# Kernel tuning notes

Hardware: AMD Instinct MI355X
Metric: run time of the kernel (lower is better)

The kernel has to match this reference:

```python
import jax, jax.numpy as jnp
import numpy as np

N_NODES = 50000
N_EDGES = 1600000
N_GRAPHS = 512
HID = 64


def _mlp_params(key, din, dout, scale=0.1):
    k1, k2, k3 = jax.random.split(key, 3)
    return (
        jax.random.normal(k1, (din, HID), jnp.float32) * scale, jnp.zeros((HID,), jnp.float32),
        jax.random.normal(k2, (HID, HID), jnp.float32) * scale, jnp.zeros((HID,), jnp.float32),
        jax.random.normal(k3, (HID, dout), jnp.float32) * scale, jnp.zeros((dout,), jnp.float32),
    )


def _mlp(x, w1, b1, w2, b2, w3, b3, out_act=None):
    h = jax.nn.relu(x @ w1 + b1)
    h = jax.nn.relu(h @ w2 + b2)
    o = h @ w3 + b3
    return o if out_act is None else out_act(o)


def setup_inputs() -> dict:
    key = jax.random.key(0)
    ks = jax.random.split(key, 8)
    nf = jax.random.normal(ks[0], (N_NODES, 1), jnp.float32)
    ef = jax.random.normal(ks[1], (N_EDGES, 1), jnp.float32)
    src = jax.random.randint(ks[2], (N_EDGES,), 0, N_NODES)
    dst = jax.random.randint(ks[3], (N_EDGES,), 0, N_NODES)
    graph_id = jnp.sort(jax.random.randint(ks[4], (N_NODES,), 0, N_GRAPHS))
    e_w1, e_b1, e_w2, e_b2, e_w3, e_b3 = _mlp_params(ks[5], 3, 1)   # edge model: [src_nf, dst_nf, ef] -> msg
    n_w1, n_b1, n_w2, n_b2, n_w3, n_b3 = _mlp_params(ks[6], 2, 1)   # node model: [nf, agg] -> unf
    m_w1, m_b1, m_w2, m_b2, m_w3, m_b3 = _mlp_params(ks[7], 1, 1)   # node-wise MLP with Sigmoid out_act
    return dict(nf=nf, ef=ef, src=src, dst=dst, graph_id=graph_id,
                e_w1=e_w1, e_b1=e_b1, e_w2=e_w2, e_b2=e_b2, e_w3=e_w3, e_b3=e_b3,
                n_w1=n_w1, n_b1=n_b1, n_w2=n_w2, n_b2=n_b2, n_w3=n_w3, n_b3=n_b3,
                m_w1=m_w1, m_b1=m_b1, m_w2=m_w2, m_b2=m_b2, m_w3=m_w3, m_b3=m_b3)


def reference(nf, ef, src, dst, graph_id,
              e_w1, e_b1, e_w2, e_b2, e_w3, e_b3,
              n_w1, n_b1, n_w2, n_b2, n_w3, n_b3,
              m_w1, m_b1, m_w2, m_b2, m_w3, m_b3):
    # MPNN layer: message on edges, sum-aggregate to dst nodes, node update
    em_in = jnp.concatenate([nf[src], nf[dst], ef], axis=-1)          # [E, 3]
    msg = _mlp(em_in, e_w1, e_b1, e_w2, e_b2, e_w3, e_b3)             # [E, 1]
    agg = jax.ops.segment_sum(msg, dst, num_segments=N_NODES)        # [N, 1]
    unf = _mlp(jnp.concatenate([nf, agg], axis=-1),
               n_w1, n_b1, n_w2, n_b2, n_w3, n_b3)                    # [N, 1]
    # node-wise MLP with Sigmoid output activation
    node_out = _mlp(unf, m_w1, m_b1, m_w2, m_b2, m_w3, m_b3,
                    out_act=jax.nn.sigmoid)                           # [N, 1]
    # sum readout per graph, then final sigmoid
    rd = jax.ops.segment_sum(node_out, graph_id, num_segments=N_GRAPHS)  # [G, 1]
    return jax.nn.sigmoid(rd)
```

## Files before the change

### kernel.cpp

```cpp
#include <hip/hip_runtime.h>
#include <math.h>

#define HID 64
#define BKT_SHIFT 13
#define BKT_RANGE 8192
#define CCHUNK 32

typedef __attribute__((ext_vector_type(8))) short short8;
typedef __attribute__((ext_vector_type(4))) float f32x4;
typedef unsigned long long ull;

union FragU {
    uint4 q;
    short8 v;
    uint32_t u[4];
};

__device__ __forceinline__ uint32_t cvt_pk_bf16(float lo, float hi) {
    uint32_t r;
    asm("v_cvt_pk_bf16_f32 %0, %1, %2" : "=v"(r) : "v"(lo), "v"(hi));
    return r;
}

__global__ __launch_bounds__(256) void edge_mlp_kernel(
    const float* __restrict__ nf, const float* __restrict__ ef,
    const int* __restrict__ src, const int* __restrict__ dst,
    const float* __restrict__ w1, const float* __restrict__ b1,
    const float* __restrict__ w2, const float* __restrict__ b2,
    const float* __restrict__ w3, const float* __restrict__ b3,
    uint2* __restrict__ recs, ull* __restrict__ offs,
    float* __restrict__ aggFb, int E, int B, int mode)
{
    __shared__ uint4 hbuf[256 * 8];

    const int tid  = threadIdx.x;
    const int lane = tid & 63;
    const int wid  = tid >> 6;
    const int g    = lane >> 4;
    const int eL   = lane & 15;

    FragU af[4][2];
#pragma unroll
    for (int t = 0; t < 4; ++t)
#pragma unroll
        for (int h = 0; h < 2; ++h)
#pragma unroll
            for (int e2 = 0; e2 < 4; ++e2) {
                int k0 = h * 32 + g * 8 + 2 * e2;
                float v0 = w2[(k0    ) * HID + t * 16 + eL];
                float v1 = w2[(k0 + 1) * HID + t * 16 + eL];
                af[t][h].u[e2] = cvt_pk_bf16(v0, v1);
            }

    float b2v[16], w3v[16];
#pragma unroll
    for (int t = 0; t < 4; ++t)
#pragma unroll
        for (int r = 0; r < 4; ++r) {
            int j = t * 16 + g * 4 + r;
            b2v[t * 4 + r] = b2[j];
            w3v[t * 4 + r] = w3[j];
        }
    const float b3c = b3[0];

    const int e0 = blockIdx.x * 256;
    const int eidx = e0 + tid;
    const int ei = eidx < E ? eidx : E - 1;
    const int dmine = dst[ei];
    {
        float a = nf[src[ei]];
        float b = nf[dmine];
        float c = ef[ei];

        uint32_t pk[32];
#pragma unroll
        for (int k2 = 0; k2 < 32; ++k2) {
            int k0 = 2 * k2, k1 = 2 * k2 + 1;
            float h0 = fmaxf(fmaf(a, w1[k0], fmaf(b, w1[HID + k0], fmaf(c, w1[2 * HID + k0], b1[k0]))), 0.f);
            float h1 = fmaxf(fmaf(a, w1[k1], fmaf(b, w1[HID + k1], fmaf(c, w1[2 * HID + k1], b1[k1]))), 0.f);
            pk[k2] = cvt_pk_bf16(h0, h1);
        }

        uint4* rowp = &hbuf[tid * 8];
        int sw = tid & 7;
#pragma unroll
        for (int ch = 0; ch < 8; ++ch)
            rowp[ch ^ sw] = make_uint4(pk[4 * ch], pk[4 * ch + 1], pk[4 * ch + 2], pk[4 * ch + 3]);
    }

    float mymsg = 0.f;

#pragma unroll
    for (int s = 0; s < 4; ++s) {
        int row = wid * 64 + s * 16 + eL;
        int sw  = lane & 7;
        FragU bf0, bf1;
        bf0.q = hbuf[row * 8 + ((    g) ^ sw)];
        bf1.q = hbuf[row * 8 + ((4 + g) ^ sw)];

        f32x4 ac[4];
#pragma unroll
        for (int t = 0; t < 4; ++t) {
            ac[t][0] = b2v[t * 4 + 0];
            ac[t][1] = b2v[t * 4 + 1];
            ac[t][2] = b2v[t * 4 + 2];
            ac[t][3] = b2v[t * 4 + 3];
            ac[t] = __builtin_amdgcn_mfma_f32_16x16x32_bf16(af[t][0].v, bf0.v, ac[t], 0, 0, 0);
            ac[t] = __builtin_amdgcn_mfma_f32_16x16x32_bf16(af[t][1].v, bf1.v, ac[t], 0, 0, 0);
        }

        float p = 0.f;
#pragma unroll
        for (int t = 0; t < 4; ++t)
#pragma unroll
            for (int r = 0; r < 4; ++r)
                p = fmaf(fmaxf(ac[t][r], 0.f), w3v[t * 4 + r], p);

        p += __shfl_xor(p, 16);
        p += __shfl_xor(p, 32);

        if (s == (lane >> 4)) mymsg = p + b3c;
    }

    const bool valid = eidx < E;

    if (mode == 1) {
        if (valid) atomicAdd(&aggFb[dmine], mymsg);
        return;
    }

    const int bkt = dmine >> BKT_SHIFT;
    const ull lt = (1ull << lane) - 1;
    int myslot = 0;
    int off = 0;
    uint32_t pack_lo = 0, pack_hi = 0;
    for (int b = 0; b < B; ++b) {
        if (b < 4) pack_lo |= (uint32_t)off << (8 * b);
        else       pack_hi |= (uint32_t)off << (8 * (b - 4));
        ull m = __ballot(valid && bkt == b);
        if (valid && bkt == b) myslot = off + (int)__popcll(m & lt);
        off += (int)__popcll(m);
    }
    pack_hi |= (uint32_t)off << 24;

    const size_t wgl = (size_t)blockIdx.x * 4 + wid;
    if (valid) recs[wgl * 64 + myslot] = make_uint2((uint32_t)dmine, __float_as_uint(mymsg));
    if (lane == 0) offs[wgl] = ((ull)pack_hi << 32) | (ull)pack_lo;
}

__global__ __launch_bounds__(256) void bucket_accum_kernel(
    const uint2* __restrict__ recs, const ull* __restrict__ offs,
    float* __restrict__ partial, int NW, int B)
{
    __shared__ float acc[BKT_RANGE];

    const int b = blockIdx.x / CCHUNK;
    const int c = blockIdx.x % CCHUNK;

    for (int i = threadIdx.x; i < BKT_RANGE; i += 256) acc[i] = 0.f;
    __syncthreads();

    const int wpc = (NW + CCHUNK - 1) / CCHUNK;
    const int w0 = c * wpc;
    const int w1 = (w0 + wpc < NW) ? w0 + wpc : NW;
    const int nb = b + 1;
    const int base_node = b << BKT_SHIFT;

    for (int w = w0 + threadIdx.x; w < w1; w += 256) {
        ull ov = offs[w];
        uint32_t lo = (uint32_t)ov, hi = (uint32_t)(ov >> 32);
        int ob = (int)(((b  < 4) ? (lo >> (8 * b))        : (hi >> (8 * (b  - 4)))) & 0xFF);
        int oe = (int)(((nb < 4) ? (lo >> (8 * nb))       : (hi >> (8 * (nb - 4)))) & 0xFF);
        const uint2* rb = recs + (size_t)w * 64;
        for (int r = ob; r < oe; ++r) {
            uint2 rec = rb[r];
            atomicAdd(&acc[(int)rec.x - base_node], __uint_as_float(rec.y));
        }
    }
    __syncthreads();

    float* pb = partial + ((size_t)b * CCHUNK + c) * BKT_RANGE;
    for (int i = threadIdx.x; i < BKT_RANGE; i += 256) pb[i] = acc[i];
}

__global__ __launch_bounds__(256) void bucket_reduce_kernel(
    const float* __restrict__ partial, float* __restrict__ agg, int N)
{
    int n = blockIdx.x * 256 + threadIdx.x;
    if (n >= N) return;
    int b = n >> BKT_SHIFT, nl = n & (BKT_RANGE - 1);
    const float* p = partial + (size_t)b * CCHUNK * BKT_RANGE + nl;
    float s = 0.f;
#pragma unroll 8
    for (int c = 0; c < CCHUNK; ++c) s += p[(size_t)c * BKT_RANGE];
    agg[n] = s;
}

__global__ __launch_bounds__(64) void node_mfma_kernel(
    const float* __restrict__ nf, const float* __restrict__ agg,
    const int* __restrict__ gid,
    const float* __restrict__ nw1, const float* __restrict__ nb1,
    const float* __restrict__ nw2, const float* __restrict__ nb2,
    const float* __restrict__ nw3, const float* __restrict__ nb3,
    const float* __restrict__ mw1, const float* __restrict__ mb1,
    const float* __restrict__ mw2, const float* __restrict__ mb2,
    const float* __restrict__ mw3, const float* __restrict__ mb3,
    float* __restrict__ rd, int N)
{
    __shared__ uint4 hbuf[64 * 8];
    __shared__ float unfbuf[64];
    __shared__ float obuf[64];

    const int lane = threadIdx.x;
    const int g    = lane >> 4;
    const int eL   = lane & 15;
    const int sw   = lane & 7;

    const int base = blockIdx.x * 64;
    const int idx  = base + lane;
    const int i    = idx < N ? idx : N - 1;
    const float x0 = nf[i];
    const float x1 = agg[i];

    {
        uint32_t pk[32];
#pragma unroll
        for (int k2 = 0; k2 < 32; ++k2) {
            int k0 = 2 * k2, k1 = 2 * k2 + 1;
            float h0 = fmaxf(fmaf(x0, nw1[k0], fmaf(x1, nw1[HID + k0], nb1[k0])), 0.f);
            float h1 = fmaxf(fmaf(x0, nw1[k1], fmaf(x1, nw1[HID + k1], nb1[k1])), 0.f);
            pk[k2] = cvt_pk_bf16(h0, h1);
        }
        uint4* rowp = &hbuf[lane * 8];
#pragma unroll
        for (int ch = 0; ch < 8; ++ch)
            rowp[ch ^ sw] = make_uint4(pk[4 * ch], pk[4 * ch + 1], pk[4 * ch + 2], pk[4 * ch + 3]);

        FragU af[4][2];
#pragma unroll
        for (int t = 0; t < 4; ++t)
#pragma unroll
            for (int h = 0; h < 2; ++h)
#pragma unroll
                for (int e2 = 0; e2 < 4; ++e2) {
                    int k0 = h * 32 + g * 8 + 2 * e2;
                    float v0 = nw2[(k0    ) * HID + t * 16 + eL];
                    float v1 = nw2[(k0 + 1) * HID + t * 16 + eL];
                    af[t][h].u[e2] = cvt_pk_bf16(v0, v1);
                }
        float b2v[16], w3v[16];
#pragma unroll
        for (int t = 0; t < 4; ++t)
#pragma unroll
            for (int r = 0; r < 4; ++r) {
                int j = t * 16 + g * 4 + r;
                b2v[t * 4 + r] = nb2[j];
                w3v[t * 4 + r] = nw3[j];
            }
        const float b3c = nb3[0];

#pragma unroll
        for (int s = 0; s < 4; ++s) {
            int row = s * 16 + eL;
            FragU bf0, bf1;
            bf0.q = hbuf[row * 8 + ((    g) ^ (row & 7))];
            bf1.q = hbuf[row * 8 + ((4 + g) ^ (row & 7))];

            f32x4 ac[4];
#pragma unroll
            for (int t = 0; t < 4; ++t) {
                ac[t][0] = b2v[t * 4 + 0];
                ac[t][1] = b2v[t * 4 + 1];
                ac[t][2] = b2v[t * 4 + 2];
                ac[t][3] = b2v[t * 4 + 3];
                ac[t] = __builtin_amdgcn_mfma_f32_16x16x32_bf16(af[t][0].v, bf0.v, ac[t], 0, 0, 0);
                ac[t] = __builtin_amdgcn_mfma_f32_16x16x32_bf16(af[t][1].v, bf1.v, ac[t], 0, 0, 0);
            }

            float p = 0.f;
#pragma unroll
            for (int t = 0; t < 4; ++t)
#pragma unroll
                for (int r = 0; r < 4; ++r)
                    p = fmaf(fmaxf(ac[t][r], 0.f), w3v[t * 4 + r], p);

            p += __shfl_xor(p, 16);
            p += __shfl_xor(p, 32);

            if (lane < 16)
                unfbuf[s * 16 + lane] = p + b3c;
        }
    }

    const float unf = unfbuf[lane];

    {
        uint32_t pk[32];
#pragma unroll
        for (int k2 = 0; k2 < 32; ++k2) {
            int k0 = 2 * k2, k1 = 2 * k2 + 1;
            float h0 = fmaxf(fmaf(unf, mw1[k0], mb1[k0]), 0.f);
            float h1 = fmaxf(fmaf(unf, mw1[k1], mb1[k1]), 0.f);
            pk[k2] = cvt_pk_bf16(h0, h1);
        }
        uint4* rowp = &hbuf[lane * 8];
#pragma unroll
        for (int ch = 0; ch < 8; ++ch)
            rowp[ch ^ sw] = make_uint4(pk[4 * ch], pk[4 * ch + 1], pk[4 * ch + 2], pk[4 * ch + 3]);

        FragU af[4][2];
#pragma unroll
        for (int t = 0; t < 4; ++t)
#pragma unroll
            for (int h = 0; h < 2; ++h)
#pragma unroll
                for (int e2 = 0; e2 < 4; ++e2) {
                    int k0 = h * 32 + g * 8 + 2 * e2;
                    float v0 = mw2[(k0    ) * HID + t * 16 + eL];
                    float v1 = mw2[(k0 + 1) * HID + t * 16 + eL];
                    af[t][h].u[e2] = cvt_pk_bf16(v0, v1);
                }
        float b2v[16], w3v[16];
#pragma unroll
        for (int t = 0; t < 4; ++t)
#pragma unroll
            for (int r = 0; r < 4; ++r) {
                int j = t * 16 + g * 4 + r;
                b2v[t * 4 + r] = mb2[j];
                w3v[t * 4 + r] = mw3[j];
            }
        const float b3c = mb3[0];

#pragma unroll
        for (int s = 0; s < 4; ++s) {
            int row = s * 16 + eL;
            FragU bf0, bf1;
            bf0.q = hbuf[row * 8 + ((    g) ^ (row & 7))];
            bf1.q = hbuf[row * 8 + ((4 + g) ^ (row & 7))];

            f32x4 ac[4];
#pragma unroll
            for (int t = 0; t < 4; ++t) {
                ac[t][0] = b2v[t * 4 + 0];
                ac[t][1] = b2v[t * 4 + 1];
                ac[t][2] = b2v[t * 4 + 2];
                ac[t][3] = b2v[t * 4 + 3];
                ac[t] = __builtin_amdgcn_mfma_f32_16x16x32_bf16(af[t][0].v, bf0.v, ac[t], 0, 0, 0);
                ac[t] = __builtin_amdgcn_mfma_f32_16x16x32_bf16(af[t][1].v, bf1.v, ac[t], 0, 0, 0);
            }

            float p = 0.f;
#pragma unroll
            for (int t = 0; t < 4; ++t)
#pragma unroll
                for (int r = 0; r < 4; ++r)
                    p = fmaf(fmaxf(ac[t][r], 0.f), w3v[t * 4 + r], p);

            p += __shfl_xor(p, 16);
            p += __shfl_xor(p, 32);

            if (lane < 16) {
                float o = p + b3c;
                obuf[s * 16 + lane] = 1.0f / (1.0f + expf(-o));
            }
        }
    }

    {
        const bool ok = idx < N;
        float v = ok ? obuf[lane] : 0.0f;
        int   gg = gid[i];

#pragma unroll
        for (int d = 1; d < 64; d <<= 1) {
            float vup = __shfl_up(v, d);
            int   gup = __shfl_up(gg, d);
            if (lane >= d && gup == gg) v += vup;
        }
        int gdn = __shfl_down(gg, 1);
        bool tail = (lane == 63) || (gdn != gg);
        if (tail)
            atomicAdd(&rd[gg], v);
    }
}

__global__ void readout_kernel(const float* __restrict__ rd,
                               float* __restrict__ out, int G)
{
    int g = blockIdx.x * blockDim.x + threadIdx.x;
    if (g < G) out[g] = 1.0f / (1.0f + expf(-rd[g]));
}

extern "C" void kernel_launch(void* const* d_in, const int* in_sizes, int n_in,
                              void* d_out, int out_size, void* d_ws, size_t ws_size,
                              hipStream_t stream)
{
    const float* nf  = (const float*)d_in[0];
    const float* ef  = (const float*)d_in[1];
    const int*   src = (const int*)  d_in[2];
    const int*   dst = (const int*)  d_in[3];
    const int*   gid = (const int*)  d_in[4];

    const float* e_w1 = (const float*)d_in[5];
    const float* e_b1 = (const float*)d_in[6];
    const float* e_w2 = (const float*)d_in[7];
    const float* e_b2 = (const float*)d_in[8];
    const float* e_w3 = (const float*)d_in[9];
    const float* e_b3 = (const float*)d_in[10];

    const float* n_w1 = (const float*)d_in[11];
    const float* n_b1 = (const float*)d_in[12];
    const float* n_w2 = (const float*)d_in[13];
    const float* n_b2 = (const float*)d_in[14];
    const float* n_w3 = (const float*)d_in[15];
    const float* n_b3 = (const float*)d_in[16];

    const float* m_w1 = (const float*)d_in[17];
    const float* m_b1 = (const float*)d_in[18];
    const float* m_w2 = (const float*)d_in[19];
    const float* m_b2 = (const float*)d_in[20];
    const float* m_w3 = (const float*)d_in[21];
    const float* m_b3 = (const float*)d_in[22];

    const int N = in_sizes[0];
    const int E = in_sizes[2];
    const int G = out_size;

    const int NW = (E + 63) / 64;
    const int B  = (N + BKT_RANGE - 1) / BKT_RANGE;

    size_t recs_b   = (size_t)NW * 64 * sizeof(uint2);
    size_t offs_b   = (size_t)NW * sizeof(ull);
    size_t part_b   = (size_t)B * CCHUNK * BKT_RANGE * sizeof(float);
    size_t need     = recs_b + offs_b + part_b + ((size_t)N + G) * sizeof(float);
    bool   bucketok = (B <= 8) && (need <= ws_size);

    float* out = (float*)d_out;

    if (bucketok) {
        uint2* recs    = (uint2*)d_ws;
        ull*   offs    = (ull*)((char*)d_ws + recs_b);
        float* partial = (float*)((char*)d_ws + recs_b + offs_b);
        float* agg     = (float*)((char*)d_ws + recs_b + offs_b + part_b);
        float* rd      = agg + N;

        hipMemsetAsync(rd, 0, (size_t)G * sizeof(float), stream);

        edge_mlp_kernel<<<(E + 255) / 256, 256, 0, stream>>>(
            nf, ef, src, dst, e_w1, e_b1, e_w2, e_b2, e_w3, e_b3,
            recs, offs, nullptr, E, B, 0);

        bucket_accum_kernel<<<B * CCHUNK, 256, 0, stream>>>(
            recs, offs, partial, NW, B);

        bucket_reduce_kernel<<<(N + 255) / 256, 256, 0, stream>>>(
            partial, agg, N);

        node_mfma_kernel<<<(N + 63) / 64, 64, 0, stream>>>(
            nf, agg, gid,
            n_w1, n_b1, n_w2, n_b2, n_w3, n_b3,
            m_w1, m_b1, m_w2, m_b2, m_w3, m_b3,
            rd, N);

        readout_kernel<<<(G + 255) / 256, 256, 0, stream>>>(rd, out, G);
    } else {
        float* agg = (float*)d_ws;
        float* rd  = agg + N;

        hipMemsetAsync(d_ws, 0, ((size_t)N + G) * sizeof(float), stream);

        edge_mlp_kernel<<<(E + 255) / 256, 256, 0, stream>>>(
            nf, ef, src, dst, e_w1, e_b1, e_w2, e_b2, e_w3, e_b3,
            nullptr, nullptr, agg, E, B, 1);

        node_mfma_kernel<<<(N + 63) / 64, 64, 0, stream>>>(
            nf, agg, gid,
            n_w1, n_b1, n_w2, n_b2, n_w3, n_b3,
            m_w1, m_b1, m_w2, m_b2, m_w3, m_b3,
            rd, N);

        readout_kernel<<<(G + 255) / 256, 256, 0, stream>>>(rd, out, G);
    }
}
```

Baseline: 85.85 us.

## Compute first MLP layer with MFMA and prepack bf16 weights in a prep kernel

```diff
diff --git a/kernel.cpp b/kernel.cpp
--- a/kernel.cpp
+++ b/kernel.cpp
@@ -21,17 +21,47 @@
     asm("v_cvt_pk_bf16_f32 %0, %1, %2" : "=v"(r) : "v"(lo), "v"(hi));
     return r;
 }
-
-__global__ __launch_bounds__(256) void edge_mlp_kernel(
+__device__ __forceinline__ float bf16lo_f(uint32_t u) { return __uint_as_float(u << 16); }
+__device__ __forceinline__ float bf16hi_f(uint32_t u) { return __uint_as_float(u & 0xFFFF0000u); }
+__device__ __forceinline__ unsigned short bf16_of(float v) {
+    return (unsigned short)(cvt_pk_bf16(v, 0.f) & 0xFFFFu);
+}
+
+__global__ void prep_kernel(
+    const float* __restrict__ w1,  const float* __restrict__ b1,  const float* __restrict__ w2,
+    const float* __restrict__ nw1, const float* __restrict__ nb1, const float* __restrict__ nw2,
+    const float* __restrict__ mw1, const float* __restrict__ mb1, const float* __restrict__ mw2,
+    unsigned short* __restrict__ w1x,  unsigned short* __restrict__ w2T,
+    unsigned short* __restrict__ nw1x, unsigned short* __restrict__ nw2T,
+    unsigned short* __restrict__ mw1x, unsigned short* __restrict__ mw2T)
+{
+    int t = blockIdx.x * 256 + threadIdx.x;
+    if (t < 4096) {
+        int j = t >> 6, k = t & 63;
+        w2T [t] = bf16_of(w2 [k * HID + j]);
+        nw2T[t] = bf16_of(nw2[k * HID + j]);
+        mw2T[t] = bf16_of(mw2[k * HID + j]);
+    }
+    if (t < 512) {
+        int j = t >> 3, k = t & 7;
+        float ve = k == 0 ? w1[j] : k == 1 ? w1[HID + j] : k == 2 ? w1[2 * HID + j] : k == 3 ? b1[j] : 0.f;
+        float vn = k == 0 ? nw1[j] : k == 1 ? nw1[HID + j] : k == 2 ? nb1[j] : 0.f;
+        float vm = k == 0 ? mw1[j] : k == 1 ? mb1[j] : 0.f;
+        w1x [t] = bf16_of(ve);
+        nw1x[t] = bf16_of(vn);
+        mw1x[t] = bf16_of(vm);
+    }
+}
+
+__global__ __launch_bounds__(256, 4) void edge_mfma2_kernel(
     const float* __restrict__ nf, const float* __restrict__ ef,
     const int* __restrict__ src, const int* __restrict__ dst,
-    const float* __restrict__ w1, const float* __restrict__ b1,
-    const float* __restrict__ w2, const float* __restrict__ b2,
-    const float* __restrict__ w3, const float* __restrict__ b3,
+    const unsigned short* __restrict__ w1x, const unsigned short* __restrict__ w2T,
+    const float* __restrict__ b2, const float* __restrict__ w3, const float* __restrict__ b3,
     uint2* __restrict__ recs, ull* __restrict__ offs,
     float* __restrict__ aggFb, int E, int B, int mode)
 {
-    __shared__ uint4 hbuf[256 * 8];
+    __shared__ uint2 tile[4][16][16];
 
     const int tid  = threadIdx.x;
     const int lane = tid & 63;
@@ -39,87 +69,80 @@
     const int g    = lane >> 4;
     const int eL   = lane & 15;
 
-    FragU af[4][2];
+    FragU af1[4];
+#pragma unroll
+    for (int t = 0; t < 4; ++t) {
+        uint4 q = *(const uint4*)&w1x[(t * 16 + eL) * 8];
+        af1[t].q = (g == 0) ? q : make_uint4(0, 0, 0, 0);
+    }
+    FragU af2[4][2];
 #pragma unroll
     for (int t = 0; t < 4; ++t)
 #pragma unroll
         for (int h = 0; h < 2; ++h)
-#pragma unroll
-            for (int e2 = 0; e2 < 4; ++e2) {
-                int k0 = h * 32 + g * 8 + 2 * e2;
-                float v0 = w2[(k0    ) * HID + t * 16 + eL];
-                float v1 = w2[(k0 + 1) * HID + t * 16 + eL];
-                af[t][h].u[e2] = cvt_pk_bf16(v0, v1);
-            }
-
-    float b2v[16], w3v[16];
-#pragma unroll
-    for (int t = 0; t < 4; ++t)
-#pragma unroll
-        for (int r = 0; r < 4; ++r) {
-            int j = t * 16 + g * 4 + r;
-            b2v[t * 4 + r] = b2[j];
-            w3v[t * 4 + r] = w3[j];
-        }
+            af2[t][h].q = *(const uint4*)&w2T[(t * 16 + eL) * 64 + h * 32 + g * 8];
+
+    f32x4 b2v4[4];
+    uint32_t w3p[8];
+#pragma unroll
+    for (int t = 0; t < 4; ++t) {
+        int j = t * 16 + g * 4;
+        b2v4[t] = *(const f32x4*)&b2[j];
+        f32x4 wv = *(const f32x4*)&w3[j];
+        w3p[2 * t]     = cvt_pk_bf16(wv[0], wv[1]);
+        w3p[2 * t + 1] = cvt_pk_bf16(wv[2], wv[3]);
+    }
     const float b3c = b3[0];
 
-    const int e0 = blockIdx.x * 256;
+    const int e0   = blockIdx.x * 256;
     const int eidx = e0 + tid;
-    const int ei = eidx < E ? eidx : E - 1;
+    const int ei   = eidx < E ? eidx : E - 1;
     const int dmine = dst[ei];
-    {
-        float a = nf[src[ei]];
-        float b = nf[dmine];
-        float c = ef[ei];
-
-        uint32_t pk[32];
-#pragma unroll
-        for (int k2 = 0; k2 < 32; ++k2) {
-            int k0 = 2 * k2, k1 = 2 * k2 + 1;
-            float h0 = fmaxf(fmaf(a, w1[k0], fmaf(b, w1[HID + k0], fmaf(c, w1[2 * HID + k0], b1[k0]))), 0.f);
-            float h1 = fmaxf(fmaf(a, w1[k1], fmaf(b, w1[HID + k1], fmaf(c, w1[2 * HID + k1], b1[k1]))), 0.f);
-            pk[k2] = cvt_pk_bf16(h0, h1);
-        }
-
-        uint4* rowp = &hbuf[tid * 8];
-        int sw = tid & 7;
-#pragma unroll
-        for (int ch = 0; ch < 8; ++ch)
-            rowp[ch ^ sw] = make_uint4(pk[4 * ch], pk[4 * ch + 1], pk[4 * ch + 2], pk[4 * ch + 3]);
-    }
+    const float a = nf[src[ei]];
+    const float b = nf[dmine];
+    const float c = ef[ei];
 
     float mymsg = 0.f;
 
 #pragma unroll
     for (int s = 0; s < 4; ++s) {
-        int row = wid * 64 + s * 16 + eL;
-        int sw  = lane & 7;
+        float av = __shfl(a, s * 16 + eL);
+        float bv = __shfl(b, s * 16 + eL);
+        float cv = __shfl(c, s * 16 + eL);
+        FragU bin;
+        bin.u[0] = (g == 0) ? cvt_pk_bf16(av, bv) : 0u;
+        bin.u[1] = (g == 0) ? cvt_pk_bf16(cv, 1.0f) : 0u;
+        bin.u[2] = 0u; bin.u[3] = 0u;
+
+#pragma unroll
+        for (int t = 0; t < 4; ++t) {
+            f32x4 h4 = __builtin_amdgcn_mfma_f32_16x16x32_bf16(
+                af1[t].v, bin.v, (f32x4){0.f, 0.f, 0.f, 0.f}, 0, 0, 0);
+            uint32_t p0 = cvt_pk_bf16(fmaxf(h4[0], 0.f), fmaxf(h4[1], 0.f));
+            uint32_t p1 = cvt_pk_bf16(fmaxf(h4[2], 0.f), fmaxf(h4[3], 0.f));
+            tile[wid][eL][(4 * t + g) ^ ((eL & 7) << 1)] = make_uint2(p0, p1);
+        }
+
         FragU bf0, bf1;
-        bf0.q = hbuf[row * 8 + ((    g) ^ sw)];
-        bf1.q = hbuf[row * 8 + ((4 + g) ^ sw)];
-
-        f32x4 ac[4];
-#pragma unroll
-        for (int t = 0; t < 4; ++t) {
-            ac[t][0] = b2v[t * 4 + 0];
-            ac[t][1] = b2v[t * 4 + 1];
-            ac[t][2] = b2v[t * 4 + 2];
-            ac[t][3] = b2v[t * 4 + 3];
-            ac[t] = __builtin_amdgcn_mfma_f32_16x16x32_bf16(af[t][0].v, bf0.v, ac[t], 0, 0, 0);
-            ac[t] = __builtin_amdgcn_mfma_f32_16x16x32_bf16(af[t][1].v, bf1.v, ac[t], 0, 0, 0);
+        {
+            const uint4* row = (const uint4*)&tile[wid][eL][0];
+            bf0.q = row[(g)     ^ (eL & 7)];
+            bf1.q = row[(4 + g) ^ (eL & 7)];
         }
 
         float p = 0.f;
 #pragma unroll
-        for (int t = 0; t < 4; ++t)
-#pragma unroll
-            for (int r = 0; r < 4; ++r)
-                p = fmaf(fmaxf(ac[t][r], 0.f), w3v[t * 4 + r], p);
-
+        for (int t = 0; t < 4; ++t) {
+            f32x4 ac = __builtin_amdgcn_mfma_f32_16x16x32_bf16(af2[t][0].v, bf0.v, b2v4[t], 0, 0, 0);
+            ac = __builtin_amdgcn_mfma_f32_16x16x32_bf16(af2[t][1].v, bf1.v, ac, 0, 0, 0);
+            p = fmaf(fmaxf(ac[0], 0.f), bf16lo_f(w3p[2 * t]),     p);
+            p = fmaf(fmaxf(ac[1], 0.f), bf16hi_f(w3p[2 * t]),     p);
+            p = fmaf(fmaxf(ac[2], 0.f), bf16lo_f(w3p[2 * t + 1]), p);
+            p = fmaf(fmaxf(ac[3], 0.f), bf16hi_f(w3p[2 * t + 1]), p);
+        }
         p += __shfl_xor(p, 16);
         p += __shfl_xor(p, 32);
-
-        if (s == (lane >> 4)) mymsg = p + b3c;
+        if (s == g) mymsg = p + b3c;
     }
 
     const bool valid = eidx < E;
@@ -169,8 +192,8 @@
     for (int w = w0 + threadIdx.x; w < w1; w += 256) {
         ull ov = offs[w];
         uint32_t lo = (uint32_t)ov, hi = (uint32_t)(ov >> 32);
-        int ob = (int)(((b  < 4) ? (lo >> (8 * b))        : (hi >> (8 * (b  - 4)))) & 0xFF);
-        int oe = (int)(((nb < 4) ? (lo >> (8 * nb))       : (hi >> (8 * (nb - 4)))) & 0xFF);
+        int ob = (int)(((b  < 4) ? (lo >> (8 * b))  : (hi >> (8 * (b  - 4)))) & 0xFF);
+        int oe = (int)(((nb < 4) ? (lo >> (8 * nb)) : (hi >> (8 * (nb - 4)))) & 0xFF);
         const uint2* rb = recs + (size_t)w * 64;
         for (int r = ob; r < oe; ++r) {
             uint2 rec = rb[r];
@@ -196,191 +219,143 @@
     agg[n] = s;
 }
 
-__global__ __launch_bounds__(64) void node_mfma_kernel(
+__global__ __launch_bounds__(64, 2) void node_mfma2_kernel(
     const float* __restrict__ nf, const float* __restrict__ agg,
     const int* __restrict__ gid,
-    const float* __restrict__ nw1, const float* __restrict__ nb1,
-    const float* __restrict__ nw2, const float* __restrict__ nb2,
-    const float* __restrict__ nw3, const float* __restrict__ nb3,
-    const float* __restrict__ mw1, const float* __restrict__ mb1,
-    const float* __restrict__ mw2, const float* __restrict__ mb2,
-    const float* __restrict__ mw3, const float* __restrict__ mb3,
+    const unsigned short* __restrict__ nw1x, const unsigned short* __restrict__ nw2T,
+    const float* __restrict__ nb2, const float* __restrict__ nw3, const float* __restrict__ nb3,
+    const unsigned short* __restrict__ mw1x, const unsigned short* __restrict__ mw2T,
+    const float* __restrict__ mb2, const float* __restrict__ mw3, const float* __restrict__ mb3,
     float* __restrict__ rd, int N)
 {
-    __shared__ uint4 hbuf[64 * 8];
-    __shared__ float unfbuf[64];
-    __shared__ float obuf[64];
+    __shared__ uint2 tile[16][16];
 
     const int lane = threadIdx.x;
     const int g    = lane >> 4;
     const int eL   = lane & 15;
-    const int sw   = lane & 7;
-
-    const int base = blockIdx.x * 64;
-    const int idx  = base + lane;
-    const int i    = idx < N ? idx : N - 1;
-    const float x0 = nf[i];
-    const float x1 = agg[i];
+
+    const int n0 = blockIdx.x * 16;
+    const int nn = n0 + eL < N ? n0 + eL : N - 1;
+    const float x0 = nf[nn];
+    const float x1 = agg[nn];
+
+    float unf, o;
 
     {
-        uint32_t pk[32];
-#pragma unroll
-        for (int k2 = 0; k2 < 32; ++k2) {
-            int k0 = 2 * k2, k1 = 2 * k2 + 1;
-            float h0 = fmaxf(fmaf(x0, nw1[k0], fmaf(x1, nw1[HID + k0], nb1[k0])), 0.f);
-            float h1 = fmaxf(fmaf(x0, nw1[k1], fmaf(x1, nw1[HID + k1], nb1[k1])), 0.f);
-            pk[k2] = cvt_pk_bf16(h0, h1);
-        }
-        uint4* rowp = &hbuf[lane * 8];
-#pragma unroll
-        for (int ch = 0; ch < 8; ++ch)
-            rowp[ch ^ sw] = make_uint4(pk[4 * ch], pk[4 * ch + 1], pk[4 * ch + 2], pk[4 * ch + 3]);
-
-        FragU af[4][2];
-#pragma unroll
-        for (int t = 0; t < 4; ++t)
+        FragU af1[4], af2[4][2];
+        f32x4 b2v4[4]; uint32_t w3p[8];
+#pragma unroll
+        for (int t = 0; t < 4; ++t) {
+            uint4 q = *(const uint4*)&nw1x[(t * 16 + eL) * 8];
+            af1[t].q = (g == 0) ? q : make_uint4(0, 0, 0, 0);
 #pragma unroll
             for (int h = 0; h < 2; ++h)
-#pragma unroll
-                for (int e2 = 0; e2 < 4; ++e2) {
-                    int k0 = h * 32 + g * 8 + 2 * e2;
-                    float v0 = nw2[(k0    ) * HID + t * 16 + eL];
-                    float v1 = nw2[(k0 + 1) * HID + t * 16 + eL];
-                    af[t][h].u[e2] = cvt_pk_bf16(v0, v1);
-                }
-        float b2v[16], w3v[16];
-#pragma unroll
-        for (int t = 0; t < 4; ++t)
-#pragma unroll
-            for (int r = 0; r < 4; ++r) {
-                int j = t * 16 + g * 4 + r;
-                b2v[t * 4 + r] = nb2[j];
-                w3v[t * 4 + r] = nw3[j];
-            }
-        const float b3c = nb3[0];
-
-#pragma unroll
-        for (int s = 0; s < 4; ++s) {
-            int row = s * 16 + eL;
-            FragU bf0, bf1;
-            bf0.q = hbuf[row * 8 + ((    g) ^ (row & 7))];
-            bf1.q = hbuf[row * 8 + ((4 + g) ^ (row & 7))];
-
-            f32x4 ac[4];
-#pragma unroll
-            for (int t = 0; t < 4; ++t) {
-                ac[t][0] = b2v[t * 4 + 0];
-                ac[t][1] = b2v[t * 4 + 1];
-                ac[t][2] = b2v[t * 4 + 2];
-                ac[t][3] = b2v[t * 4 + 3];
-                ac[t] = __builtin_amdgcn_mfma_f32_16x16x32_bf16(af[t][0].v, bf0.v, ac[t], 0, 0, 0);
-                ac[t] = __builtin_amdgcn_mfma_f32_16x16x32_bf16(af[t][1].v, bf1.v, ac[t], 0, 0, 0);
-            }
-
-            float p = 0.f;
-#pragma unroll
-            for (int t = 0; t < 4; ++t)
-#pragma unroll
-                for (int r = 0; r < 4; ++r)
-                    p = fmaf(fmaxf(ac[t][r], 0.f), w3v[t * 4 + r], p);
-
-            p += __shfl_xor(p, 16);
-            p += __shfl_xor(p, 32);
-
-            if (lane < 16)
-                unfbuf[s * 16 + lane] = p + b3c;
-        }
-    }
-
-    const float unf = unfbuf[lane];
+                af2[t][h].q = *(const uint4*)&nw2T[(t * 16 + eL) * 64 + h * 32 + g * 8];
+            int j = t * 16 + g * 4;
+            b2v4[t] = *(const f32x4*)&nb2[j];
+            f32x4 wv = *(const f32x4*)&nw3[j];
+            w3p[2 * t]     = cvt_pk_bf16(wv[0], wv[1]);
+            w3p[2 * t + 1] = cvt_pk_bf16(wv[2], wv[3]);
+        }
+        FragU bin;
+        bin.u[0] = (g == 0) ? cvt_pk_bf16(x0, x1) : 0u;
+        bin.u[1] = (g == 0) ? cvt_pk_bf16(1.0f, 0.f) : 0u;
+        bin.u[2] = 0u; bin.u[3] = 0u;
+
+#pragma unroll
+        for (int t = 0; t < 4; ++t) {
+            f32x4 h4 = __builtin_amdgcn_mfma_f32_16x16x32_bf16(
+                af1[t].v, bin.v, (f32x4){0.f, 0.f, 0.f, 0.f}, 0, 0, 0);
+            uint32_t p0 = cvt_pk_bf16(fmaxf(h4[0], 0.f), fmaxf(h4[1], 0.f));
+            uint32_t p1 = cvt_pk_bf16(fmaxf(h4[2], 0.f), fmaxf(h4[3], 0.f));
+            tile[eL][(4 * t + g) ^ ((eL & 7) << 1)] = make_uint2(p0, p1);
+        }
+        FragU bf0, bf1;
+        {
+            const uint4* row = (const uint4*)&tile[eL][0];
+            bf0.q = row[(g)     ^ (eL & 7)];
+            bf1.q = row[(4 + g) ^ (eL & 7)];
+        }
+        float p = 0.f;
+#pragma unroll
+        for (int t = 0; t < 4; ++t) {
+            f32x4 ac = __builtin_amdgcn_mfma_f32_16x16x32_bf16(af2[t][0].v, bf0.v, b2v4[t], 0, 0, 0);
+            ac = __builtin_amdgcn_mfma_f32_16x16x32_bf16(af2[t][1].v, bf1.v, ac, 0, 0, 0);
+            p = fmaf(fmaxf(ac[0], 0.f), bf16lo_f(w3p[2 * t]),     p);
+            p = fmaf(fmaxf(ac[1], 0.f), bf16hi_f(w3p[2 * t]),     p);
+            p = fmaf(fmaxf(ac[2], 0.f), bf16lo_f(w3p[2 * t + 1]), p);
+            p = fmaf(fmaxf(ac[3], 0.f), bf16hi_f(w3p[2 * t + 1]), p);
+        }
+        p += __shfl_xor(p, 16);
+        p += __shfl_xor(p, 32);
+        unf = p + nb3[0];
+    }
 
     {
-        uint32_t pk[32];
-#pragma unroll
-        for (int k2 = 0; k2 < 32; ++k2) {
-            int k0 = 2 * k2, k1 = 2 * k2 + 1;
-            float h0 = fmaxf(fmaf(unf, mw1[k0], mb1[k0]), 0.f);
-            float h1 = fmaxf(fmaf(unf, mw1[k1], mb1[k1]), 0.f);
-            pk[k2] = cvt_pk_bf16(h0, h1);
-        }
-        uint4* rowp = &hbuf[lane * 8];
-#pragma unroll
-        for (int ch = 0; ch < 8; ++ch)
-            rowp[ch ^ sw] = make_uint4(pk[4 * ch], pk[4 * ch + 1], pk[4 * ch + 2], pk[4 * ch + 3]);
-
-        FragU af[4][2];
-#pragma unroll
-        for (int t = 0; t < 4; ++t)
+        FragU af1[4], af2[4][2];
+        f32x4 b2v4[4]; uint32_t w3p[8];
+#pragma unroll
+        for (int t = 0; t < 4; ++t) {
+            uint4 q = *(const uint4*)&mw1x[(t * 16 + eL) * 8];
+            af1[t].q = (g == 0) ? q : make_uint4(0, 0, 0, 0);
 #pragma unroll
             for (int h = 0; h < 2; ++h)
-#pragma unroll
-                for (int e2 = 0; e2 < 4; ++e2) {
-                    int k0 = h * 32 + g * 8 + 2 * e2;
-                    float v0 = mw2[(k0    ) * HID + t * 16 + eL];
-                    float v1 = mw2[(k0 + 1) * HID + t * 16 + eL];
-                    af[t][h].u[e2] = cvt_pk_bf16(v0, v1);
-                }
-        float b2v[16], w3v[16];
-#pragma unroll
-        for (int t = 0; t < 4; ++t)
-#pragma unroll
-            for (int r = 0; r < 4; ++r) {
-                int j = t * 16 + g * 4 + r;
-                b2v[t * 4 + r] = mb2[j];
-                w3v[t * 4 + r] = mw3[j];
-            }
-        const float b3c = mb3[0];
-
-#pragma unroll
-        for (int s = 0; s < 4; ++s) {
-            int row = s * 16 + eL;
-            FragU bf0, bf1;
-            bf0.q = hbuf[row * 8 + ((    g) ^ (row & 7))];
-            bf1.q = hbuf[row * 8 + ((4 + g) ^ (row & 7))];
-
-            f32x4 ac[4];
-#pragma unroll
-            for (int t = 0; t < 4; ++t) {
-                ac[t][0] = b2v[t * 4 + 0];
-                ac[t][1] = b2v[t * 4 + 1];
-                ac[t][2] = b2v[t * 4 + 2];
-                ac[t][3] = b2v[t * 4 + 3];
-                ac[t] = __builtin_amdgcn_mfma_f32_16x16x32_bf16(af[t][0].v, bf0.v, ac[t], 0, 0, 0);
-                ac[t] = __builtin_amdgcn_mfma_f32_16x16x32_bf16(af[t][1].v, bf1.v, ac[t], 0, 0, 0);
-            }
-
-            float p = 0.f;
-#pragma unroll
-            for (int t = 0; t < 4; ++t)
-#pragma unroll
-                for (int r = 0; r < 4; ++r)
-                    p = fmaf(fmaxf(ac[t][r], 0.f), w3v[t * 4 + r], p);
-
-            p += __shfl_xor(p, 16);
-            p += __shfl_xor(p, 32);
-
-            if (lane < 16) {
-                float o = p + b3c;
-                obuf[s * 16 + lane] = 1.0f / (1.0f + expf(-o));
-            }
-        }
-    }
+                af2[t][h].q = *(const uint4*)&mw2T[(t * 16 + eL) * 64 + h * 32 + g * 8];
+            int j = t * 16 + g * 4;
+            b2v4[t] = *(const f32x4*)&mb2[j];
+            f32x4 wv = *(const f32x4*)&mw3[j];
+            w3p[2 * t]     = cvt_pk_bf16(wv[0], wv[1]);
+            w3p[2 * t + 1] = cvt_pk_bf16(wv[2], wv[3]);
+        }
+        FragU bin;
+        bin.u[0] = (g == 0) ? cvt_pk_bf16(unf, 1.0f) : 0u;
+        bin.u[1] = 0u; bin.u[2] = 0u; bin.u[3] = 0u;
+
+#pragma unroll
+        for (int t = 0; t < 4; ++t) {
+            f32x4 h4 = __builtin_amdgcn_mfma_f32_16x16x32_bf16(
+                af1[t].v, bin.v, (f32x4){0.f, 0.f, 0.f, 0.f}, 0, 0, 0);
+            uint32_t p0 = cvt_pk_bf16(fmaxf(h4[0], 0.f), fmaxf(h4[1], 0.f));
+            uint32_t p1 = cvt_pk_bf16(fmaxf(h4[2], 0.f), fmaxf(h4[3], 0.f));
+            tile[eL][(4 * t + g) ^ ((eL & 7) << 1)] = make_uint2(p0, p1);
+        }
+        FragU bf0, bf1;
+        {
+            const uint4* row = (const uint4*)&tile[eL][0];
+            bf0.q = row[(g)     ^ (eL & 7)];
+            bf1.q = row[(4 + g) ^ (eL & 7)];
+        }
+        float p = 0.f;
+#pragma unroll
+        for (int t = 0; t < 4; ++t) {
+            f32x4 ac = __builtin_amdgcn_mfma_f32_16x16x32_bf16(af2[t][0].v, bf0.v, b2v4[t], 0, 0, 0);
+            ac = __builtin_amdgcn_mfma_f32_16x16x32_bf16(af2[t][1].v, bf1.v, ac, 0, 0, 0);
+            p = fmaf(fmaxf(ac[0], 0.f), bf16lo_f(w3p[2 * t]),     p);
+            p = fmaf(fmaxf(ac[1], 0.f), bf16hi_f(w3p[2 * t]),     p);
+            p = fmaf(fmaxf(ac[2], 0.f), bf16lo_f(w3p[2 * t + 1]), p);
+            p = fmaf(fmaxf(ac[3], 0.f), bf16hi_f(w3p[2 * t + 1]), p);
+        }
+        p += __shfl_xor(p, 16);
+        p += __shfl_xor(p, 32);
+        o = p + mb3[0];
+    }
+
+    float node_out = 1.0f / (1.0f + expf(-o));
 
     {
-        const bool ok = idx < N;
-        float v = ok ? obuf[lane] : 0.0f;
-        int   gg = gid[i];
-
-#pragma unroll
-        for (int d = 1; d < 64; d <<= 1) {
+        int gg = gid[nn];
+        float v = (n0 + eL < N && g == 0) ? node_out : 0.f;
+#pragma unroll
+        for (int d = 1; d < 16; d <<= 1) {
             float vup = __shfl_up(v, d);
             int   gup = __shfl_up(gg, d);
-            if (lane >= d && gup == gg) v += vup;
-        }
-        int gdn = __shfl_down(gg, 1);
-        bool tail = (lane == 63) || (gdn != gg);
-        if (tail)
-            atomicAdd(&rd[gg], v);
+            if (lane >= d && lane < 16 && gup == gg) v += vup;
+        }
+        if (lane < 16 && n0 + lane < N) {
+            int gdn = __shfl_down(gg, 1);
+            bool tail = (lane == 15) || (n0 + lane + 1 >= N) || (gdn != gg);
+            if (tail) atomicAdd(&rd[gg], v);
+        }
     }
 }
 
@@ -429,25 +404,38 @@
     const int NW = (E + 63) / 64;
     const int B  = (N + BKT_RANGE - 1) / BKT_RANGE;
 
-    size_t recs_b   = (size_t)NW * 64 * sizeof(uint2);
-    size_t offs_b   = (size_t)NW * sizeof(ull);
-    size_t part_b   = (size_t)B * CCHUNK * BKT_RANGE * sizeof(float);
-    size_t need     = recs_b + offs_b + part_b + ((size_t)N + G) * sizeof(float);
-    bool   bucketok = (B <= 8) && (need <= ws_size);
+    size_t wts_b  = 32 * 1024;
+    size_t recs_b = (size_t)NW * 64 * sizeof(uint2);
+    size_t offs_b = (size_t)NW * sizeof(ull);
+    size_t part_b = (size_t)B * CCHUNK * BKT_RANGE * sizeof(float);
+    size_t need   = wts_b + recs_b + offs_b + part_b + ((size_t)N + G) * sizeof(float);
+    bool bucketok = (B <= 8) && (need <= ws_size);
+
+    char* wp = (char*)d_ws;
+    unsigned short* w1x  = (unsigned short*)(wp);
+    unsigned short* nw1x = (unsigned short*)(wp + 1024);
+    unsigned short* mw1x = (unsigned short*)(wp + 2048);
+    unsigned short* w2T  = (unsigned short*)(wp + 4096);
+    unsigned short* nw2T = (unsigned short*)(wp + 4096 + 8192);
+    unsigned short* mw2T = (unsigned short*)(wp + 4096 + 16384);
 
     float* out = (float*)d_out;
 
+    prep_kernel<<<16, 256, 0, stream>>>(
+        e_w1, e_b1, e_w2, n_w1, n_b1, n_w2, m_w1, m_b1, m_w2,
+        w1x, w2T, nw1x, nw2T, mw1x, mw2T);
+
     if (bucketok) {
-        uint2* recs    = (uint2*)d_ws;
-        ull*   offs    = (ull*)((char*)d_ws + recs_b);
-        float* partial = (float*)((char*)d_ws + recs_b + offs_b);
-        float* agg     = (float*)((char*)d_ws + recs_b + offs_b + part_b);
+        uint2* recs    = (uint2*)(wp + wts_b);
+        ull*   offs    = (ull*)(wp + wts_b + recs_b);
+        float* partial = (float*)(wp + wts_b + recs_b + offs_b);
+        float* agg     = (float*)(wp + wts_b + recs_b + offs_b + part_b);
         float* rd      = agg + N;
 
         hipMemsetAsync(rd, 0, (size_t)G * sizeof(float), stream);
 
-        edge_mlp_kernel<<<(E + 255) / 256, 256, 0, stream>>>(
-            nf, ef, src, dst, e_w1, e_b1, e_w2, e_b2, e_w3, e_b3,
+        edge_mfma2_kernel<<<(E + 255) / 256, 256, 0, stream>>>(
+            nf, ef, src, dst, w1x, w2T, e_b2, e_w3, e_b3,
             recs, offs, nullptr, E, B, 0);
 
         bucket_accum_kernel<<<B * CCHUNK, 256, 0, stream>>>(
@@ -456,27 +444,27 @@
         bucket_reduce_kernel<<<(N + 255) / 256, 256, 0, stream>>>(
             partial, agg, N);
 
-        node_mfma_kernel<<<(N + 63) / 64, 64, 0, stream>>>(
+        node_mfma2_kernel<<<(N + 15) / 16, 64, 0, stream>>>(
             nf, agg, gid,
-            n_w1, n_b1, n_w2, n_b2, n_w3, n_b3,
-            m_w1, m_b1, m_w2, m_b2, m_w3, m_b3,
+            nw1x, nw2T, n_b2, n_w3, n_b3,
+            mw1x, mw2T, m_b2, m_w3, m_b3,
             rd, N);
 
         readout_kernel<<<(G + 255) / 256, 256, 0, stream>>>(rd, out, G);
     } else {
-        float* agg = (float*)d_ws;
+        float* agg = (float*)(wp + wts_b);
         float* rd  = agg + N;
 
-        hipMemsetAsync(d_ws, 0, ((size_t)N + G) * sizeof(float), stream);
-
-        edge_mlp_kernel<<<(E + 255) / 256, 256, 0, stream>>>(
-            nf, ef, src, dst, e_w1, e_b1, e_w2, e_b2, e_w3, e_b3,
+        hipMemsetAsync(agg, 0, ((size_t)N + G) * sizeof(float), stream);
+
+        edge_mfma2_kernel<<<(E + 255) / 256, 256, 0, stream>>>(
+            nf, ef, src, dst, w1x, w2T, e_b2, e_w3, e_b3,
             nullptr, nullptr, agg, E, B, 1);
 
-        node_mfma_kernel<<<(N + 63) / 64, 64, 0, stream>>>(
+        node_mfma2_kernel<<<(N + 15) / 16, 64, 0, stream>>>(
             nf, agg, gid,
-            n_w1, n_b1, n_w2, n_b2, n_w3, n_b3,
-            m_w1, m_b1, m_w2, m_b2, m_w3, m_b3,
+            nw1x, nw2T, n_b2, n_w3, n_b3,
+            mw1x, mw2T, m_b2, m_w3, m_b3,
             rd, N);
 
         readout_kernel<<<(G + 255) / 256, 256, 0, stream>>>(rd, out, G);
```

Result: no change. 87.40 us (+1.8%).
